# Performance work log

Measured on AMD Instinct MI355X. Metric: run time of the kernel, lower is better.

The kernel has to match this reference:

```python
import jax, jax.numpy as jnp
import numpy as np

# Constants from the source's eval path
BBOX_STDS = (0.1, 0.1, 0.2, 0.2)   # cfg.TRAIN.BBOX_NORMALIZE_STDS (MEANS are zeros)
PRE_NMS = 300                       # cfg.TEST.RPN_POST_NMS_TOP_N
POST_K = 100                        # cfg.PERSON_NMS (fixed output size; zero-padded)
NMS_THRESH = 0.3
SCORE_THRESH = 0.05


def setup_inputs() -> dict:
    key = jax.random.key(0)
    k1, k2, k3, k4 = jax.random.split(key, 4)
    B, N = 64, 32768
    H = W = 1024.0
    # plausible RPN proposal boxes inside the image
    xy = jax.random.uniform(k1, (B, N, 2)) * (W - 160.0)
    wh = jax.random.uniform(k2, (B, N, 2)) * 120.0 + 8.0
    boxes = jnp.concatenate([xy, xy + wh], axis=-1)          # [B,N,4] x1y1x2y2
    cls_prob = jax.random.uniform(k3, (B, N, 2))              # softmax probs [bg, person]
    box_deltas = jax.random.normal(k4, (B, N, 4)) * 0.5
    im_info = jnp.tile(jnp.array([H, W, 1.0], jnp.float32), (B, 1))
    return {"cls_prob": cls_prob, "boxes": boxes, "box_deltas": box_deltas, "im_info": im_info}


def _decode_and_clip(boxes, deltas, im_info):
    # bbox_transform_inv with de-normalized deltas, then clip_boxes
    stds = jnp.array(BBOX_STDS, boxes.dtype)
    d = deltas * stds                                         # MEANS are zero
    w = boxes[..., 2] - boxes[..., 0] + 1.0
    h = boxes[..., 3] - boxes[..., 1] + 1.0
    cx = boxes[..., 0] + 0.5 * w
    cy = boxes[..., 1] + 0.5 * h
    pcx = d[..., 0] * w + cx
    pcy = d[..., 1] * h + cy
    pw = jnp.exp(d[..., 2]) * w
    ph = jnp.exp(d[..., 3]) * h
    x1 = pcx - 0.5 * pw
    y1 = pcy - 0.5 * ph
    x2 = pcx + 0.5 * pw
    y2 = pcy + 0.5 * ph
    hmax = im_info[:, 0][:, None] - 1.0   # [B,1]
    wmax = im_info[:, 1][:, None] - 1.0
    x1 = jnp.clip(x1, 0.0, wmax)
    y1 = jnp.clip(y1, 0.0, hmax)
    x2 = jnp.clip(x2, 0.0, wmax)
    y2 = jnp.clip(y2, 0.0, hmax)
    return jnp.stack([x1, y1, x2, y2], axis=-1)               # [B,N,4]


def _nms_single(boxes_i, scores_i):
    # threshold -> sort (top-k) -> greedy NMS -> fixed-size padded output
    valid = scores_i >= SCORE_THRESH
    s = jnp.where(valid, scores_i, -jnp.inf)
    topv, topi = jax.lax.top_k(s, PRE_NMS)                    # descending sort + pre_nms_topN
    b = boxes_i[topi]                                          # [M,4]
    x1, y1, x2, y2 = b[:, 0], b[:, 1], b[:, 2], b[:, 3]
    areas = (x2 - x1 + 1.0) * (y2 - y1 + 1.0)
    xx1 = jnp.maximum(x1[:, None], x1[None, :])
    yy1 = jnp.maximum(y1[:, None], y1[None, :])
    xx2 = jnp.minimum(x2[:, None], x2[None, :])
    yy2 = jnp.minimum(y2[:, None], y2[None, :])
    inter = jnp.maximum(xx2 - xx1 + 1.0, 0.0) * jnp.maximum(yy2 - yy1 + 1.0, 0.0)
    iou = inter / (areas[:, None] + areas[None, :] - inter)    # [M,M]
    iou = jax.lax.stop_gradient(iou)                           # only drives the boolean keep mask
    idx = jnp.arange(PRE_NMS)
    keep0 = jnp.isfinite(topv)                                 # drop below-threshold padding

    def body(i, keep):
        sup = (iou[i] > NMS_THRESH) & (idx > i) & keep[i]
        return keep & ~sup

    keep = jax.lax.fori_loop(0, PRE_NMS, body, keep0)
    # compact kept boxes (in score order) into a fixed [POST_K,4] buffer, zero-padded
    rank = jnp.cumsum(keep) - 1
    dst = jnp.where(keep & (rank < POST_K), rank, POST_K)      # overflow row POST_K is discarded
    out = jnp.zeros((POST_K + 1, 4), b.dtype).at[dst].set(b)
    return out[:POST_K]


def reference(cls_prob, boxes, box_deltas, im_info):
    pred = _decode_and_clip(boxes, box_deltas, im_info)        # [B,N,4]
    scores_person = cls_prob[:, :, 1]                          # person column
    kept = jax.vmap(_nms_single)(pred, scores_person)          # [B,POST_K,4]
    B = pred.shape[0]
    bidx = jnp.broadcast_to(jnp.arange(B, dtype=pred.dtype)[:, None, None], (B, POST_K, 1))
    return jnp.concatenate([bidx, kept], axis=-1)              # [B,POST_K,5] rois
```

## Files before the change

kernel.cpp:

```cpp
#include <hip/hip_runtime.h>
#include <cstdint>
#include <cstddef>

#define PRE_NMS  300
#define POST_K   100
#define NBUCKET  4096
#define CAND_MAX 2048
#define NCHUNK   16
#define SUB      128
#define NWORDS   5
#define SUP_STRIDE 8
#define NMS_T    0.3f
#define SCORE_T  0.05f
#define FAST_T   0.9875f

typedef unsigned long long u64;

__global__ __launch_bounds__(256) void scan_kernel(
    const float* __restrict__ cls_prob,
    u64* __restrict__ candG,
    int* __restrict__ cntG,
    int N)
{
    const int b     = blockIdx.x >> 4;
    const int chunk = blockIdx.x & (NCHUNK - 1);
    const int nq    = N / 2;
    const int per   = (nq + NCHUNK - 1) / NCHUNK;
    const int base  = chunk * per;
    const int end   = min(base + per, nq);

    __shared__ int lcnt;
    __shared__ u64 lbuf[SUB];
    if (threadIdx.x == 0) lcnt = 0;
    __syncthreads();

    const float4* cp = (const float4*)(cls_prob + (size_t)b * N * 2);
    for (int q = base + threadIdx.x; q < end; q += 256) {
        float4 v = cp[q];
        #pragma unroll
        for (int h = 0; h < 2; ++h) {
            float s = h ? v.w : v.y;
            if (s >= FAST_T) {
                int pos = atomicAdd(&lcnt, 1);
                if (pos < SUB) {
                    unsigned int m = __float_as_uint(s) ^ 0xFFFFFFFFu;
                    lbuf[pos] = ((u64)m << 32) | (unsigned int)(2 * q + h);
                }
            }
        }
    }
    __syncthreads();

    const int cnt = lcnt;
    u64* cb = candG + ((size_t)b * NCHUNK + chunk) * SUB;
    for (int i = threadIdx.x; i < min(cnt, SUB); i += 256) cb[i] = lbuf[i];
    if (threadIdx.x == 0) cntG[b * NCHUNK + chunk] = cnt;
}

__device__ __forceinline__ u64 keep_init_word(int Kv, int w) {
    int rem = Kv - 64 * w;
    if (rem >= 64) return ~0ull;
    if (rem <= 0)  return 0ull;
    return (1ull << rem) - 1ull;
}

__device__ __forceinline__ u64 bits_above(int b) {
    return (b == 63) ? 0ull : (~0ull << (b + 1));
}

__global__ __launch_bounds__(512) void proposal_kernel(
    const float* __restrict__ cls_prob,
    const float* __restrict__ boxes,
    const float* __restrict__ deltas,
    const float* __restrict__ im_info,
    float* __restrict__ out,
    const u64* __restrict__ candG,
    const int* __restrict__ cntG,
    int useWS, int N)
{
    const int b   = blockIdx.x;
    const int tid = threadIdx.x;
    const int NT  = 512;

    __shared__ u64 cand[CAND_MAX];
    int* hist = (int*)cand;
    __shared__ float4 bb[PRE_NMS];
    __shared__ u64 supRow[PRE_NMS * SUP_STRIDE];
    __shared__ u64 keepw[NWORDS];
    __shared__ int sel[POST_K];
    __shared__ int n_out;
    __shared__ int sh_cc;
    __shared__ int sh_ok;
    __shared__ int cand_count;
    __shared__ int cutoff;
    __shared__ int ccnt[NCHUNK], coff[NCHUNK + 1];

    if (tid == 0) cand_count = 0;
    __syncthreads();

    const float4* cp = (const float4*)(cls_prob + (size_t)b * N * 2);
    const int nq = N / 2;

    if (useWS && tid < NCHUNK) ccnt[tid] = cntG[b * NCHUNK + tid];
    __syncthreads();
    if (tid == 0) {
        int ok = useWS;
        int tot = 0;
        if (useWS) {
            for (int c = 0; c < NCHUNK; ++c) {
                if (ccnt[c] > SUB) ok = 0;
                coff[c] = tot;
                tot += ccnt[c];
            }
            coff[NCHUNK] = tot;
            if (tot < PRE_NMS || tot > CAND_MAX) ok = 0;
        }
        sh_ok = ok;
        sh_cc = tot;
    }
    __syncthreads();
    const bool fast = (sh_ok != 0);
    int cc;

    if (fast) {
        cc = sh_cc;
        const int c = tid >> 5;
        const u64* cb = candG + ((size_t)b * NCHUNK + c) * SUB;
        const int n = ccnt[c], o = coff[c];
        for (int i = tid & 31; i < n; i += 32) cand[o + i] = cb[i];
    } else {
        for (int q = tid; q < nq; q += NT) {
            float4 v = cp[q];
            #pragma unroll
            for (int h = 0; h < 2; ++h) {
                float s = h ? v.w : v.y;
                if (s >= FAST_T) {
                    int pos = atomicAdd(&cand_count, 1);
                    if (pos < CAND_MAX) {
                        unsigned int m = __float_as_uint(s) ^ 0xFFFFFFFFu;
                        cand[pos] = ((u64)m << 32) | (unsigned int)(2 * q + h);
                    }
                }
            }
        }
        __syncthreads();
        if (cand_count < PRE_NMS) {
            for (int i = tid; i < NBUCKET; i += NT) hist[i] = 0;
            __syncthreads();
            for (int q = tid; q < nq; q += NT) {
                float4 v = cp[q];
                if (v.y >= SCORE_T) atomicAdd(&hist[min((int)(v.y * (float)NBUCKET), NBUCKET - 1)], 1);
                if (v.w >= SCORE_T) atomicAdd(&hist[min((int)(v.w * (float)NBUCKET), NBUCKET - 1)], 1);
            }
            __syncthreads();
            if (tid == 0) {
                int acc = 0, c = 0;
                for (int i = NBUCKET - 1; i >= 0; --i) {
                    acc += hist[i];
                    if (acc >= PRE_NMS) { c = i; break; }
                }
                cutoff = c;
                cand_count = 0;
            }
            __syncthreads();
            const int c = cutoff;
            for (int q = tid; q < nq; q += NT) {
                float4 v = cp[q];
                #pragma unroll
                for (int h = 0; h < 2; ++h) {
                    float s = h ? v.w : v.y;
                    if (s >= SCORE_T) {
                        int bu = min((int)(s * (float)NBUCKET), NBUCKET - 1);
                        if (bu >= c) {
                            int pos = atomicAdd(&cand_count, 1);
                            if (pos < CAND_MAX) {
                                unsigned int m = __float_as_uint(s) ^ 0xFFFFFFFFu;
                                cand[pos] = ((u64)m << 32) | (unsigned int)(2 * q + h);
                            }
                        }
                    }
                }
            }
            __syncthreads();
        }
        cc = min(cand_count, CAND_MAX);
        if (tid == 0) sh_cc = cc;
        __syncthreads();
        cc = sh_cc;
    }

    for (int k = tid; k < PRE_NMS; k += NT) bb[k] = make_float4(0.f, 0.f, 0.f, 0.f);
    __syncthreads();

    const int Kv = min(cc, PRE_NMS);

    const float hmax = im_info[b * 3 + 0] - 1.0f;
    const float wmax = im_info[b * 3 + 1] - 1.0f;
    for (int c = tid; c < cc; c += NT) {
        u64 my = cand[c];
        int idx = (int)(my & 0xFFFFFFFFull);
        float4 bo = *(const float4*)(boxes  + ((size_t)b * N + idx) * 4);
        float4 de = *(const float4*)(deltas + ((size_t)b * N + idx) * 4);
        int rank = 0;
        int k = 0;
        for (; k + 8 <= cc; k += 8) {
            u64 q0 = cand[k];     u64 q1 = cand[k + 1];
            u64 q2 = cand[k + 2]; u64 q3 = cand[k + 3];
            u64 q4 = cand[k + 4]; u64 q5 = cand[k + 5];
            u64 q6 = cand[k + 6]; u64 q7 = cand[k + 7];
            rank += (int)(q0 < my) + (int)(q1 < my) + (int)(q2 < my) + (int)(q3 < my)
                  + (int)(q4 < my) + (int)(q5 < my) + (int)(q6 < my) + (int)(q7 < my);
        }
        for (; k < cc; ++k) rank += (cand[k] < my) ? 1 : 0;
        if (rank < PRE_NMS) {
            float w  = bo.z - bo.x + 1.0f;
            float hh = bo.w - bo.y + 1.0f;
            float cx = bo.x + 0.5f * w;
            float cy = bo.y + 0.5f * hh;
            float pcx = de.x * 0.1f * w + cx;
            float pcy = de.y * 0.1f * hh + cy;
            float pw  = expf(de.z * 0.2f) * w;
            float ph  = expf(de.w * 0.2f) * hh;
            float x1 = fminf(fmaxf(pcx - 0.5f * pw, 0.0f), wmax);
            float y1 = fminf(fmaxf(pcy - 0.5f * ph, 0.0f), hmax);
            float x2 = fminf(fmaxf(pcx + 0.5f * pw, 0.0f), wmax);
            float y2 = fminf(fmaxf(pcy + 0.5f * ph, 0.0f), hmax);
            bb[rank] = make_float4(x1, y1, x2, y2);
        }
    }
    __syncthreads();

    for (int t = tid; t < PRE_NMS * NWORDS; t += NT) {
        int w = t / PRE_NMS;
        int i = t - w * PRE_NMS;
        int jbase = w * 64;
        int jend  = min(jbase + 64, PRE_NMS);
        u64 bits = 0;
        int jstart = max(jbase, i + 1);
        if (jstart < jend) {
            float4 bi = bb[i];
            float ai = (bi.z - bi.x + 1.0f) * (bi.w - bi.y + 1.0f);
            for (int j = jstart; j < jend; ++j) {
                float4 bj = bb[j];
                float aj = (bj.z - bj.x + 1.0f) * (bj.w - bj.y + 1.0f);
                float xx1 = fmaxf(bi.x, bj.x);
                float yy1 = fmaxf(bi.y, bj.y);
                float xx2 = fminf(bi.z, bj.z);
                float yy2 = fminf(bi.w, bj.w);
                float iw = fmaxf(xx2 - xx1 + 1.0f, 0.0f);
                float ih = fmaxf(yy2 - yy1 + 1.0f, 0.0f);
                float inter = iw * ih;
                float iou = inter / (ai + aj - inter);
                if (iou > NMS_T) bits |= (1ull << (j - jbase));
            }
        }
        supRow[i * SUP_STRIDE + w] = bits;
    }
    __syncthreads();

    if (tid < 64) {
        u64 kw0 = keep_init_word(Kv, 0);
        u64 kw1 = keep_init_word(Kv, 1);
        u64 kw2 = keep_init_word(Kv, 2);
        u64 kw3 = keep_init_word(Kv, 3);
        u64 kw4 = keep_init_word(Kv, 4);

        int nk = 0;
        #pragma unroll
        for (int wi = 0; wi < NWORDS; ++wi) {
            if (nk >= POST_K) break;
            u64 w = (wi == 0) ? kw0 : (wi == 1) ? kw1 : (wi == 2) ? kw2 : (wi == 3) ? kw3 : kw4;
            while (w != 0ull && nk < POST_K) {
                int b1 = __ffsll(w) - 1;
                u64 w1 = w & bits_above(b1);
                int b2 = (w1 != 0ull) ? (__ffsll(w1) - 1) : -1;
                u64 w2 = (b2 >= 0) ? (w1 & bits_above(b2)) : 0ull;
                int b3 = (w2 != 0ull) ? (__ffsll(w2) - 1) : -1;
                u64 w3 = (b3 >= 0) ? (w2 & bits_above(b3)) : 0ull;
                int b4 = (w3 != 0ull) ? (__ffsll(w3) - 1) : -1;

                const int base = wi * 64;
                const u64* p1 = supRow + (size_t)(base + b1) * SUP_STRIDE;
                const u64* p2 = supRow + (size_t)(base + ((b2 >= 0) ? b2 : b1)) * SUP_STRIDE;
                const u64* p3 = supRow + (size_t)(base + ((b3 >= 0) ? b3 : b1)) * SUP_STRIDE;
                const u64* p4 = supRow + (size_t)(base + ((b4 >= 0) ? b4 : b1)) * SUP_STRIDE;
                u64 a0 = p1[0], a1 = p1[1], a2 = p1[2], a3 = p1[3], a4 = p1[4];
                u64 c0 = p2[0], c1 = p2[1], c2 = p2[2], c3 = p2[3], c4 = p2[4];
                u64 d0 = p3[0], d1 = p3[1], d2 = p3[2], d3 = p3[3], d4 = p3[4];
                u64 e0 = p4[0], e1 = p4[1], e2 = p4[2], e3 = p4[3], e4 = p4[4];

                u64 aw = (wi == 0) ? a0 : (wi == 1) ? a1 : (wi == 2) ? a2 : (wi == 3) ? a3 : a4;
                u64 cw = (wi == 0) ? c0 : (wi == 1) ? c1 : (wi == 2) ? c2 : (wi == 3) ? c3 : c4;
                u64 dw = (wi == 0) ? d0 : (wi == 1) ? d1 : (wi == 2) ? d2 : (wi == 3) ? d3 : d4;

                kw0 &= ~a0; kw1 &= ~a1; kw2 &= ~a2; kw3 &= ~a3; kw4 &= ~a4;
                ++nk;
                bool k2 = false, k3 = false;
                if (b2 >= 0 && nk < POST_K && !((aw >> b2) & 1ull)) {
                    kw0 &= ~c0; kw1 &= ~c1; kw2 &= ~c2; kw3 &= ~c3; kw4 &= ~c4;
                    ++nk; k2 = true;
                }
                if (b3 >= 0 && nk < POST_K && !((aw >> b3) & 1ull)
                    && !(k2 && ((cw >> b3) & 1ull))) {
                    kw0 &= ~d0; kw1 &= ~d1; kw2 &= ~d2; kw3 &= ~d3; kw4 &= ~d4;
                    ++nk; k3 = true;
                }
                if (b4 >= 0 && nk < POST_K && !((aw >> b4) & 1ull)
                    && !(k2 && ((cw >> b4) & 1ull))
                    && !(k3 && ((dw >> b4) & 1ull))) {
                    kw0 &= ~e0; kw1 &= ~e1; kw2 &= ~e2; kw3 &= ~e3; kw4 &= ~e4;
                    ++nk;
                }
                int blast = (b4 >= 0) ? b4 : ((b3 >= 0) ? b3 : ((b2 >= 0) ? b2 : b1));
                u64 self = (wi == 0) ? kw0 : (wi == 1) ? kw1 : (wi == 2) ? kw2 : (wi == 3) ? kw3 : kw4;
                w = self & bits_above(blast);
            }
        }
        if (tid == 0) {
            keepw[0] = kw0; keepw[1] = kw1; keepw[2] = kw2; keepw[3] = kw3; keepw[4] = kw4;
            n_out = nk;
        }
    }
    __syncthreads();

    if (tid < PRE_NMS) {
        int wi = tid >> 6, bi = tid & 63;
        u64 w = keepw[wi];
        int prefix = 0;
        #pragma unroll
        for (int ww = 0; ww < NWORDS; ++ww)
            if (ww < wi) prefix += __popcll(keepw[ww]);
        prefix += __popcll(w & ((1ull << bi) - 1ull));
        if (((w >> bi) & 1ull) && prefix < POST_K) sel[prefix] = tid;
    }
    __syncthreads();

    if (tid < POST_K) {
        float* op = out + ((size_t)b * POST_K + tid) * 5;
        op[0] = (float)b;
        if (tid < n_out) {
            float4 v = bb[sel[tid]];
            op[1] = v.x; op[2] = v.y; op[3] = v.z; op[4] = v.w;
        } else {
            op[1] = 0.0f; op[2] = 0.0f; op[3] = 0.0f; op[4] = 0.0f;
        }
    }
}

extern "C" void kernel_launch(void* const* d_in, const int* in_sizes, int n_in,
                              void* d_out, int out_size, void* d_ws, size_t ws_size,
                              hipStream_t stream) {
    const float* cls_prob = (const float*)d_in[0];
    const float* boxes    = (const float*)d_in[1];
    const float* deltas   = (const float*)d_in[2];
    const float* im_info  = (const float*)d_in[3];
    float* out = (float*)d_out;

    const int B = in_sizes[3] / 3;
    const int N = in_sizes[0] / (B * 2);

    int* cntG   = (int*)d_ws;
    u64* candG  = (u64*)((char*)d_ws + 16384);
    size_t need = 16384 + (size_t)B * NCHUNK * SUB * sizeof(u64);
    int useWS   = (ws_size >= need && B * NCHUNK * (int)sizeof(int) <= 16384) ? 1 : 0;

    if (useWS) {
        scan_kernel<<<B * NCHUNK, 256, 0, stream>>>(cls_prob, candG, cntG, N);
    }
    proposal_kernel<<<B, 512, 0, stream>>>(cls_prob, boxes, deltas, im_info, out,
                                           candG, cntG, useWS, N);
}
```

Before: 142.8 us.

## Bucket-sort candidates for ranking and compute IoU mask with wavefront ballots

On the fast path, candidate keys are bucketed by score bits into a shared histogram, prefix-scanned and scattered, then ranked only within each bucket. This replaces the all-pairs rank comparison over up to 2048 candidates. Decoding now runs one thread per top-300 slot. The IoU suppression mask is built with one wavefront per row and one lane per column, using ballots and a division-free comparison. This adds several block barriers and aliases shared buffers, and the bucket split depends on how scores fall into the float bit ranges.

```diff
diff --git a/kernel.cpp b/kernel.cpp
--- a/kernel.cpp
+++ b/kernel.cpp
@@ -10,6 +10,8 @@
 #define SUB      128
 #define NWORDS   5
 #define SUP_STRIDE 8
+#define NBUK     512
+#define MBASE    0xC0800000u
 #define NMS_T    0.3f
 #define SCORE_T  0.05f
 #define FAST_T   0.9875f
@@ -66,6 +68,14 @@
 
 __device__ __forceinline__ u64 bits_above(int b) {
     return (b == 63) ? 0ull : (~0ull << (b + 1));
+}
+
+__device__ __forceinline__ int key_bucket(u64 key) {
+    unsigned int m = (unsigned int)(key >> 32);
+    int d = (int)(m - MBASE);
+    if (d < 0) return 0;
+    int bu = d >> 9;
+    return (bu > NBUK - 1) ? (NBUK - 1) : bu;
 }
 
 __global__ __launch_bounds__(512) void proposal_kernel(
@@ -83,11 +93,16 @@
     const int NT  = 512;
 
     __shared__ u64 cand[CAND_MAX];
-    int* hist = (int*)cand;
+    int* hist4k = (int*)cand;
     __shared__ float4 bb[PRE_NMS];
+    int* buk_off = (int*)bb;
+    int* buk_cnt = buk_off + NBUK;
     __shared__ u64 supRow[PRE_NMS * SUP_STRIDE];
+    u64* skey2 = supRow;
+    __shared__ u64 skey[PRE_NMS];
     __shared__ u64 keepw[NWORDS];
     __shared__ int sel[POST_K];
+    __shared__ int ws8[8];
     __shared__ int n_out;
     __shared__ int sh_cc;
     __shared__ int sh_ok;
@@ -128,6 +143,48 @@
         const u64* cb = candG + ((size_t)b * NCHUNK + c) * SUB;
         const int n = ccnt[c], o = coff[c];
         for (int i = tid & 31; i < n; i += 32) cand[o + i] = cb[i];
+        __syncthreads();
+
+        for (int i = tid; i < NBUK; i += NT) { buk_off[i] = 0; buk_cnt[i] = 0; }
+        __syncthreads();
+        for (int c2 = tid; c2 < cc; c2 += NT)
+            atomicAdd(&buk_off[key_bucket(cand[c2])], 1);
+        __syncthreads();
+        {
+            int v = buk_off[tid];
+            int lane = tid & 63;
+            int incl = v;
+            #pragma unroll
+            for (int d = 1; d < 64; d <<= 1) {
+                int nv = __shfl_up(incl, d, 64);
+                if (lane >= d) incl += nv;
+            }
+            if (lane == 63) ws8[tid >> 6] = incl;
+            __syncthreads();
+            int woff = 0;
+            #pragma unroll
+            for (int w = 0; w < 8; ++w)
+                if (w < (tid >> 6)) woff += ws8[w];
+            __syncthreads();
+            buk_off[tid] = woff + incl - v;
+        }
+        __syncthreads();
+        for (int c2 = tid; c2 < cc; c2 += NT) {
+            u64 my = cand[c2];
+            int bu = key_bucket(my);
+            int slot = buk_off[bu] + atomicAdd(&buk_cnt[bu], 1);
+            skey2[slot] = my;
+        }
+        __syncthreads();
+        for (int s = tid; s < cc; s += NT) {
+            u64 my = skey2[s];
+            int bu = key_bucket(my);
+            int o = buk_off[bu], n = buk_cnt[bu];
+            int r = o;
+            for (int t = o; t < o + n; ++t) r += (skey2[t] < my) ? 1 : 0;
+            if (r < PRE_NMS) skey[r] = my;
+        }
+        __syncthreads();
     } else {
         for (int q = tid; q < nq; q += NT) {
             float4 v = cp[q];
@@ -145,18 +202,18 @@
         }
         __syncthreads();
         if (cand_count < PRE_NMS) {
-            for (int i = tid; i < NBUCKET; i += NT) hist[i] = 0;
+            for (int i = tid; i < NBUCKET; i += NT) hist4k[i] = 0;
             __syncthreads();
             for (int q = tid; q < nq; q += NT) {
                 float4 v = cp[q];
-                if (v.y >= SCORE_T) atomicAdd(&hist[min((int)(v.y * (float)NBUCKET), NBUCKET - 1)], 1);
-                if (v.w >= SCORE_T) atomicAdd(&hist[min((int)(v.w * (float)NBUCKET), NBUCKET - 1)], 1);
+                if (v.y >= SCORE_T) atomicAdd(&hist4k[min((int)(v.y * (float)NBUCKET), NBUCKET - 1)], 1);
+                if (v.w >= SCORE_T) atomicAdd(&hist4k[min((int)(v.w * (float)NBUCKET), NBUCKET - 1)], 1);
             }
             __syncthreads();
             if (tid == 0) {
                 int acc = 0, c = 0;
                 for (int i = NBUCKET - 1; i >= 0; --i) {
-                    acc += hist[i];
+                    acc += hist4k[i];
                     if (acc >= PRE_NMS) { c = i; break; }
                 }
                 cutoff = c;
@@ -187,32 +244,24 @@
         if (tid == 0) sh_cc = cc;
         __syncthreads();
         cc = sh_cc;
-    }
-
-    for (int k = tid; k < PRE_NMS; k += NT) bb[k] = make_float4(0.f, 0.f, 0.f, 0.f);
-    __syncthreads();
+        for (int c2 = tid; c2 < cc; c2 += NT) {
+            u64 my = cand[c2];
+            int r = 0;
+            for (int k = 0; k < cc; ++k) r += (cand[k] < my) ? 1 : 0;
+            if (r < PRE_NMS) skey[r] = my;
+        }
+        __syncthreads();
+    }
 
     const int Kv = min(cc, PRE_NMS);
 
     const float hmax = im_info[b * 3 + 0] - 1.0f;
     const float wmax = im_info[b * 3 + 1] - 1.0f;
-    for (int c = tid; c < cc; c += NT) {
-        u64 my = cand[c];
-        int idx = (int)(my & 0xFFFFFFFFull);
-        float4 bo = *(const float4*)(boxes  + ((size_t)b * N + idx) * 4);
-        float4 de = *(const float4*)(deltas + ((size_t)b * N + idx) * 4);
-        int rank = 0;
-        int k = 0;
-        for (; k + 8 <= cc; k += 8) {
-            u64 q0 = cand[k];     u64 q1 = cand[k + 1];
-            u64 q2 = cand[k + 2]; u64 q3 = cand[k + 3];
-            u64 q4 = cand[k + 4]; u64 q5 = cand[k + 5];
-            u64 q6 = cand[k + 6]; u64 q7 = cand[k + 7];
-            rank += (int)(q0 < my) + (int)(q1 < my) + (int)(q2 < my) + (int)(q3 < my)
-                  + (int)(q4 < my) + (int)(q5 < my) + (int)(q6 < my) + (int)(q7 < my);
-        }
-        for (; k < cc; ++k) rank += (cand[k] < my) ? 1 : 0;
-        if (rank < PRE_NMS) {
+    if (tid < PRE_NMS) {
+        if (tid < Kv) {
+            int idx = (int)(skey[tid] & 0xFFFFFFFFull);
+            float4 bo = *(const float4*)(boxes  + ((size_t)b * N + idx) * 4);
+            float4 de = *(const float4*)(deltas + ((size_t)b * N + idx) * 4);
             float w  = bo.z - bo.x + 1.0f;
             float hh = bo.w - bo.y + 1.0f;
             float cx = bo.x + 0.5f * w;
@@ -225,36 +274,48 @@
             float y1 = fminf(fmaxf(pcy - 0.5f * ph, 0.0f), hmax);
             float x2 = fminf(fmaxf(pcx + 0.5f * pw, 0.0f), wmax);
             float y2 = fminf(fmaxf(pcy + 0.5f * ph, 0.0f), hmax);
-            bb[rank] = make_float4(x1, y1, x2, y2);
-        }
-    }
-    __syncthreads();
-
-    for (int t = tid; t < PRE_NMS * NWORDS; t += NT) {
-        int w = t / PRE_NMS;
-        int i = t - w * PRE_NMS;
-        int jbase = w * 64;
-        int jend  = min(jbase + 64, PRE_NMS);
-        u64 bits = 0;
-        int jstart = max(jbase, i + 1);
-        if (jstart < jend) {
+            bb[tid] = make_float4(x1, y1, x2, y2);
+        } else {
+            bb[tid] = make_float4(0.f, 0.f, 0.f, 0.f);
+        }
+    }
+    __syncthreads();
+
+    {
+        const int lane = tid & 63;
+        const int wv   = tid >> 6;
+        float4 cb[5]; float ca[5];
+        #pragma unroll
+        for (int g = 0; g < 5; ++g) {
+            int j = g * 64 + lane;
+            float4 v = bb[(j < PRE_NMS) ? j : (PRE_NMS - 1)];
+            cb[g] = v;
+            ca[g] = (v.z - v.x + 1.0f) * (v.w - v.y + 1.0f);
+        }
+        for (int i = wv; i < PRE_NMS; i += 8) {
             float4 bi = bb[i];
             float ai = (bi.z - bi.x + 1.0f) * (bi.w - bi.y + 1.0f);
-            for (int j = jstart; j < jend; ++j) {
-                float4 bj = bb[j];
-                float aj = (bj.z - bj.x + 1.0f) * (bj.w - bj.y + 1.0f);
-                float xx1 = fmaxf(bi.x, bj.x);
-                float yy1 = fmaxf(bi.y, bj.y);
-                float xx2 = fminf(bi.z, bj.z);
-                float yy2 = fminf(bi.w, bj.w);
-                float iw = fmaxf(xx2 - xx1 + 1.0f, 0.0f);
-                float ih = fmaxf(yy2 - yy1 + 1.0f, 0.0f);
-                float inter = iw * ih;
-                float iou = inter / (ai + aj - inter);
-                if (iou > NMS_T) bits |= (1ull << (j - jbase));
-            }
-        }
-        supRow[i * SUP_STRIDE + w] = bits;
+            const int wi = i >> 6, bbit = i & 63;
+            u64* rp = supRow + (size_t)i * SUP_STRIDE;
+            #pragma unroll
+            for (int g = 0; g < 5; ++g) {
+                u64 word = 0;
+                if (g >= wi) {
+                    int j = g * 64 + lane;
+                    float xx1 = fmaxf(bi.x, cb[g].x);
+                    float yy1 = fmaxf(bi.y, cb[g].y);
+                    float xx2 = fminf(bi.z, cb[g].z);
+                    float yy2 = fminf(bi.w, cb[g].w);
+                    float iw = fmaxf(xx2 - xx1 + 1.0f, 0.0f);
+                    float ih = fmaxf(yy2 - yy1 + 1.0f, 0.0f);
+                    float inter = iw * ih;
+                    bool ov = (inter > NMS_T * (ai + ca[g] - inter)) && (j < PRE_NMS);
+                    u64 bal = __ballot(ov);
+                    word = (g == wi) ? (bal & bits_above(bbit)) : bal;
+                }
+                if (lane == 0) rp[g] = word;
+            }
+        }
     }
     __syncthreads();
 
```

After: 134.3 us. 1.06x faster.
